# Kernel tuning notes

Hardware: AMD Instinct MI355X
Metric: run time of the kernel (lower is better)

The kernel has to match this reference:

```python
import jax, jax.numpy as jnp
import numpy as np

K = 16
RADIUS = 0.5
LOSS_NORM = 1


def setup_inputs() -> dict:
    key = jax.random.key(0)
    k1, k2 = jax.random.split(key)
    B, N = 2, 8192
    pc = jax.random.normal(k1, (B, N, 3), dtype=jnp.float32)
    flow = jax.random.normal(k2, (B, N, 3), dtype=jnp.float32)
    return {"pc": pc, "flow": flow}


def _ball_query(pc, radius, k):
    """pc: (B,N,3) -> idx (B,N,k) int32. For each query point, the first k
    (in index order) points within radius; empty slots padded with the first
    found index (the query point itself is always in-ball at distance 0),
    matching the pointnet2 CUDA ball_query semantics."""
    B, N, _ = pc.shape
    sq = jnp.sum(pc * pc, axis=-1)  # (B,N)
    # squared pairwise distances via gram matrix: (B,N,N)
    d2 = sq[:, :, None] + sq[:, None, :] - 2.0 * jnp.einsum("bnd,bmd->bnm", pc, pc)
    within = d2 < (radius * radius)
    j = jnp.arange(N, dtype=jnp.int32)
    sentinel = jnp.int32(-2 * N)
    # key = -j for in-ball points, sentinel otherwise; top_k picks smallest j first
    keys = jnp.where(within, -j, sentinel)  # (B,N,N)
    vals, _ = jax.lax.top_k(keys, k)  # (B,N,k)
    idx = -vals
    valid = idx < N
    idx = jnp.where(valid, idx, idx[..., :1])  # pad with first neighbor (self)
    return idx


def reference(pc, flow):
    idx = _ball_query(pc, RADIUS, K)  # (B,N,K)
    # gather neighbor flows: (B,N,K,3)
    nn_flow = jax.vmap(lambda f, i: f[i])(flow, idx)
    diff = flow[:, :, None, :] - nn_flow  # (B,N,K,3)
    if LOSS_NORM == 1:
        norms = jnp.sum(jnp.abs(diff), axis=-1)
    else:
        norms = jnp.sqrt(jnp.sum(diff * diff, axis=-1))
    return jnp.mean(norms)
```

## Files before the change

### kernel.cpp

```cpp
#include <hip/hip_runtime.h>
#include <hip/hip_fp16.h>


#define NQ   8192
#define NB   2
#define KNN  16
#define QPB  64
#define WAVES 8
#define THREADS (QPB * WAVES)
#define NBQ (NB * NQ)
#define GROUPS (NBQ / QPB)
#define SLICES 4
#define SL_PAIRS 1024
#define WPP 128
#define IDXROW 130

static __device__ __forceinline__ unsigned pkrtz_u(float a, float b) {
    return __builtin_bit_cast(unsigned, __builtin_amdgcn_cvt_pkrtz(a, b));
}
static __device__ __forceinline__ __half2 u_as_h2(unsigned u) {
    return __builtin_bit_cast(__half2, u);
}
static __device__ __forceinline__ void bq_pair(unsigned xu, unsigned yu,
                                               unsigned zu, unsigned cu,
                                               __half2 qpx, __half2 qpy,
                                               __half2 qpz, __half2 q2p,
                                               unsigned& mm) {
    __half2 acc = __hsub2(u_as_h2(cu), q2p);
    acc = __hfma2(u_as_h2(xu), qpx, acc);
    acc = __hfma2(u_as_h2(yu), qpy, acc);
    acc = __hfma2(u_as_h2(zu), qpz, acc);
    mm = (__builtin_bit_cast(unsigned, acc) & 0x80008000u) | (mm >> 1);
}

__global__ __launch_bounds__(THREADS, 8)
void ballq_scan(const float* __restrict__ pc,
                unsigned short* __restrict__ wsIdx,
                unsigned char* __restrict__ wsCnt)
{
    __shared__ __align__(16) unsigned lx[SL_PAIRS];
    __shared__ __align__(16) unsigned ly[SL_PAIRS];
    __shared__ __align__(16) unsigned lz[SL_PAIRS];
    __shared__ __align__(16) unsigned lc[SL_PAIRS];
    __shared__ unsigned short s_idx[QPB][IDXROW];
    __shared__ unsigned char  s_cnt[QPB][12];

    const int tid = threadIdx.x;
    const int q   = tid & 63;
    const int c   = tid >> 6;
    const int s   = blockIdx.x & 3;
    const int g   = blockIdx.x >> 2;
    const int b   = g >> 7;
    const int i   = (g & 127) * QPB + q;

    const float* __restrict__ pcb = pc + (size_t)b * NQ * 3;
    const float2* __restrict__ f2 = (const float2*)pcb;

    for (int p = tid; p < SL_PAIRS; p += THREADS) {
        const int gp = s * SL_PAIRS + p;
        const float2 v0 = f2[3 * gp + 0];
        const float2 v1 = f2[3 * gp + 1];
        const float2 v2 = f2[3 * gp + 2];
        lx[p] = pkrtz_u(v0.x, v1.y);
        ly[p] = pkrtz_u(v0.y, v2.x);
        lz[p] = pkrtz_u(v1.x, v2.y);
        const float ne = v0.x * v0.x + v0.y * v0.y + v1.x * v1.x;
        const float no = v1.y * v1.y + v2.x * v2.x + v2.y * v2.y;
        lc[p] = pkrtz_u(0.125f - 0.5f * ne, 0.125f - 0.5f * no);
    }

    const float qx = pcb[i * 3 + 0];
    const float qy = pcb[i * 3 + 1];
    const float qz = pcb[i * 3 + 2];
    const __half2 qpx = u_as_h2(pkrtz_u(qx, qx));
    const __half2 qpy = u_as_h2(pkrtz_u(qy, qy));
    const __half2 qpz = u_as_h2(pkrtz_u(qz, qz));
    const float q2 = 0.5f * (qx * qx + qy * qy + qz * qz);
    const __half2 q2p = u_as_h2(pkrtz_u(q2, q2));

    __syncthreads();

    int cnt = 0;
    for (int r = 0; r < WPP / 64 && cnt < KNN; ++r) {
        const int pbase = c * WPP + r * 64;
        unsigned m[4] = {0u, 0u, 0u, 0u};
#pragma unroll
        for (int g4 = 0; g4 < 4; ++g4) {
#pragma unroll
            for (int w = 0; w < 4; ++w) {
                const int pb = pbase + w * 16 + g4 * 4;
                const uint4 X = *(const uint4*)&lx[pb];
                const uint4 Y = *(const uint4*)&ly[pb];
                const uint4 Z = *(const uint4*)&lz[pb];
                const uint4 C = *(const uint4*)&lc[pb];
                bq_pair(X.x, Y.x, Z.x, C.x, qpx, qpy, qpz, q2p, m[w]);
                bq_pair(X.y, Y.y, Z.y, C.y, qpx, qpy, qpz, q2p, m[w]);
                bq_pair(X.z, Y.z, Z.z, C.z, qpx, qpy, qpz, q2p, m[w]);
                bq_pair(X.w, Y.w, Z.w, C.w, qpx, qpy, qpz, q2p, m[w]);
            }
        }
        if ((m[0] & m[1] & m[2] & m[3]) == 0xFFFFFFFFu) continue;
        const unsigned h0 = ~m[0], h1 = ~m[1], h2m = ~m[2], h3 = ~m[3];

        unsigned long long ev =
              (unsigned long long)(h0 & 0xFFFFu)
            | ((unsigned long long)(h1 & 0xFFFFu) << 16)
            | ((unsigned long long)(h2m & 0xFFFFu) << 32)
            | ((unsigned long long)(h3 & 0xFFFFu) << 48);
        unsigned long long od =
              (unsigned long long)(h0 >> 16)
            | ((unsigned long long)(h1 >> 16) << 16)
            | ((unsigned long long)(h2m >> 16) << 32)
            | ((unsigned long long)(h3 >> 16) << 48);

        const int jb = s * (2 * SL_PAIRS) + 2 * pbase;
        while ((ev | od) && cnt < KNN) {
            const int pe = ev ? __builtin_ctzll(ev) : 127;
            const int po = od ? __builtin_ctzll(od) : 127;
            int j;
            if (pe <= po) { j = jb + 2 * pe;     ev &= ev - 1; }
            else          { j = jb + 2 * po + 1; od &= od - 1; }
            s_idx[q][c * KNN + cnt] = (unsigned short)j;
            ++cnt;
        }
    }
    s_cnt[q][c] = (unsigned char)cnt;
    __syncthreads();

    if (c == 0) {
        const int qid = g * QPB + q;
        unsigned short* __restrict__ rp =
            wsIdx + ((size_t)s * NBQ + qid) * KNN;
        int outc = 0;
        for (int c2 = 0; c2 < WAVES && outc < KNN; ++c2) {
            const int f = s_cnt[q][c2];
            const int take = f < (KNN - outc) ? f : (KNN - outc);
            for (int t = 0; t < take; ++t)
                rp[outc++] = s_idx[q][c2 * KNN + t];
        }
        wsCnt[qid * 4 + s] = (unsigned char)outc;
    }
}

__global__ __launch_bounds__(256)
void ballq_loss(const float* __restrict__ flow,
                const unsigned short* __restrict__ wsIdx,
                const unsigned char* __restrict__ wsCnt,
                float* __restrict__ partial)
{
    const int tid = blockIdx.x * 256 + threadIdx.x;
    const int qid = tid >> 4;
    const int t   = tid & 15;
    const int b   = qid >> 13;
    const int iq  = qid & (NQ - 1);
    const float* __restrict__ flb = flow + (size_t)b * NQ * 3;

    const unsigned cw = *(const unsigned*)(wsCnt + qid * 4);
    const int b0 = cw & 0xFF;
    const int b1 = (cw >> 8)  & 0xFF;
    const int b2 = (cw >> 16) & 0xFF;
    const int c1 = b0, c2c = b0 + b1, c3 = b0 + b1 + b2;
    int tot = c3 + ((cw >> 24) & 0xFF);
    if (tot > KNN) tot = KNN;

    const int seff = (t < tot) ? t : 0;
    const int sl   = (seff >= c1) + (seff >= c2c) + (seff >= c3);
    const int cum  = (sl == 0) ? 0 : (sl == 1) ? c1 : (sl == 2) ? c2c : c3;
    int j = wsIdx[((size_t)sl * NBQ + qid) * KNN + (seff - cum)];
    if (tot == 0) j = iq;

    const float fx = flb[iq * 3 + 0];
    const float fy = flb[iq * 3 + 1];
    const float fz = flb[iq * 3 + 2];
    float l = fabsf(fx - flb[j * 3 + 0]) +
              fabsf(fy - flb[j * 3 + 1]) +
              fabsf(fz - flb[j * 3 + 2]);

    for (int o = 32; o > 0; o >>= 1)
        l += __shfl_down(l, o, 64);
    __shared__ float sred[4];
    if ((threadIdx.x & 63) == 0) sred[threadIdx.x >> 6] = l;
    __syncthreads();
    if (threadIdx.x == 0)
        partial[blockIdx.x] = sred[0] + sred[1] + sred[2] + sred[3];
}

__global__ __launch_bounds__(1024)
void ballq_final(const float* __restrict__ partial, float* __restrict__ out)
{
    const int tid = threadIdx.x;
    float v = partial[tid];
    for (int o = 32; o > 0; o >>= 1)
        v += __shfl_down(v, o, 64);
    __shared__ float s[16];
    if ((tid & 63) == 0) s[tid >> 6] = v;
    __syncthreads();
    if (tid == 0) {
        float t = 0.0f;
#pragma unroll
        for (int w = 0; w < 16; ++w) t += s[w];
        out[0] = t * (1.0f / ((float)NB * NQ * KNN));
    }
}

extern "C" void kernel_launch(void* const* d_in, const int* in_sizes, int n_in,
                              void* d_out, int out_size, void* d_ws, size_t ws_size,
                              hipStream_t stream)
{
    (void)in_sizes; (void)n_in; (void)out_size; (void)ws_size;
    const float* pc   = (const float*)d_in[0];
    const float* flow = (const float*)d_in[1];
    float* out = (float*)d_out;

    unsigned short* wsIdx = (unsigned short*)d_ws;
    unsigned char*  wsCnt = (unsigned char*)d_ws + (size_t)SLICES * NBQ * KNN * 2;
    float* partial = (float*)(wsCnt + (size_t)NBQ * 4);

    ballq_scan<<<GROUPS * SLICES, THREADS, 0, stream>>>(pc, wsIdx, wsCnt);
    ballq_loss<<<NBQ * 16 / 256, 256, 0, stream>>>(flow, wsIdx, wsCnt, partial);
    ballq_final<<<1, 1024, 0, stream>>>(partial, out);
}
```

Before: 33.47 us.

## Transpose ball-query scan: lanes hold candidates, broadcast queries via readlane and ballot

Changes the scan so each lane keeps two candidate point pairs in registers and loops over the 64 queries of its wave, broadcasting each query with readlane and collecting in-ball masks with ballot. Each lane keeps the mask for its own query. This drops the shared-memory staging of candidates and the early-exit per 64-point round, and removes LDS reads from the inner loop. In exchange it always runs all 64 query iterations with two ballots per candidate word and per-lane select bookkeeping, so it loses the chance to stop scanning once 16 neighbors are found.

```diff
diff --git a/kernel.cpp b/kernel.cpp
--- a/kernel.cpp
+++ b/kernel.cpp
@@ -21,122 +21,104 @@
 static __device__ __forceinline__ __half2 u_as_h2(unsigned u) {
     return __builtin_bit_cast(__half2, u);
 }
-static __device__ __forceinline__ void bq_pair(unsigned xu, unsigned yu,
-                                               unsigned zu, unsigned cu,
-                                               __half2 qpx, __half2 qpy,
-                                               __half2 qpz, __half2 q2p,
-                                               unsigned& mm) {
-    __half2 acc = __hsub2(u_as_h2(cu), q2p);
-    acc = __hfma2(u_as_h2(xu), qpx, acc);
-    acc = __hfma2(u_as_h2(yu), qpy, acc);
-    acc = __hfma2(u_as_h2(zu), qpz, acc);
-    mm = (__builtin_bit_cast(unsigned, acc) & 0x80008000u) | (mm >> 1);
-}
 
 __global__ __launch_bounds__(THREADS, 8)
 void ballq_scan(const float* __restrict__ pc,
                 unsigned short* __restrict__ wsIdx,
                 unsigned char* __restrict__ wsCnt)
 {
-    __shared__ __align__(16) unsigned lx[SL_PAIRS];
-    __shared__ __align__(16) unsigned ly[SL_PAIRS];
-    __shared__ __align__(16) unsigned lz[SL_PAIRS];
-    __shared__ __align__(16) unsigned lc[SL_PAIRS];
     __shared__ unsigned short s_idx[QPB][IDXROW];
     __shared__ unsigned char  s_cnt[QPB][12];
 
     const int tid = threadIdx.x;
-    const int q   = tid & 63;
+    const int l   = tid & 63;
     const int c   = tid >> 6;
     const int s   = blockIdx.x & 3;
     const int g   = blockIdx.x >> 2;
     const int b   = g >> 7;
-    const int i   = (g & 127) * QPB + q;
 
     const float* __restrict__ pcb = pc + (size_t)b * NQ * 3;
     const float2* __restrict__ f2 = (const float2*)pcb;
 
-    for (int p = tid; p < SL_PAIRS; p += THREADS) {
-        const int gp = s * SL_PAIRS + p;
-        const float2 v0 = f2[3 * gp + 0];
-        const float2 v1 = f2[3 * gp + 1];
-        const float2 v2 = f2[3 * gp + 2];
-        lx[p] = pkrtz_u(v0.x, v1.y);
-        ly[p] = pkrtz_u(v0.y, v2.x);
-        lz[p] = pkrtz_u(v1.x, v2.y);
-        const float ne = v0.x * v0.x + v0.y * v0.y + v1.x * v1.x;
-        const float no = v1.y * v1.y + v2.x * v2.x + v2.y * v2.y;
-        lc[p] = pkrtz_u(0.125f - 0.5f * ne, 0.125f - 0.5f * no);
-    }
-
+    const int i = (g & 127) * QPB + l;
     const float qx = pcb[i * 3 + 0];
     const float qy = pcb[i * 3 + 1];
     const float qz = pcb[i * 3 + 2];
-    const __half2 qpx = u_as_h2(pkrtz_u(qx, qx));
-    const __half2 qpy = u_as_h2(pkrtz_u(qy, qy));
-    const __half2 qpz = u_as_h2(pkrtz_u(qz, qz));
-    const float q2 = 0.5f * (qx * qx + qy * qy + qz * qz);
-    const __half2 q2p = u_as_h2(pkrtz_u(q2, q2));
-
-    __syncthreads();
+    const unsigned Qx = pkrtz_u(qx, qx);
+    const unsigned Qy = pkrtz_u(qy, qy);
+    const unsigned Qz = pkrtz_u(qz, qz);
+    const float q2f = 0.5f * (qx * qx + qy * qy + qz * qz);
+    const unsigned Q2 = pkrtz_u(q2f, q2f);
+
+    const int pbase = s * SL_PAIRS + c * WPP;
+    unsigned X[2], Y[2], Z[2], C[2];
+#pragma unroll
+    for (int w = 0; w < 2; ++w) {
+        const int p = pbase + w * 64 + l;
+        const float2 v0 = f2[3 * p + 0];
+        const float2 v1 = f2[3 * p + 1];
+        const float2 v2 = f2[3 * p + 2];
+        X[w] = pkrtz_u(v0.x, v1.y);
+        Y[w] = pkrtz_u(v0.y, v2.x);
+        Z[w] = pkrtz_u(v1.x, v2.y);
+        const float ne = v0.x * v0.x + v0.y * v0.y + v1.x * v1.x;
+        const float no = v1.y * v1.y + v2.x * v2.x + v2.y * v2.y;
+        C[w] = pkrtz_u(0.125f - 0.5f * ne, 0.125f - 0.5f * no);
+    }
+
+    unsigned mevlo[2] = {0u, 0u}, mevhi[2] = {0u, 0u};
+    unsigned modlo[2] = {0u, 0u}, modhi[2] = {0u, 0u};
+    for (int qq = 0; qq < 64; ++qq) {
+        const unsigned sqx = (unsigned)__builtin_amdgcn_readlane((int)Qx, qq);
+        const unsigned sqy = (unsigned)__builtin_amdgcn_readlane((int)Qy, qq);
+        const unsigned sqz = (unsigned)__builtin_amdgcn_readlane((int)Qz, qq);
+        const unsigned sq2 = (unsigned)__builtin_amdgcn_readlane((int)Q2, qq);
+        const bool own = (l == qq);
+#pragma unroll
+        for (int w = 0; w < 2; ++w) {
+            __half2 acc = __hsub2(u_as_h2(C[w]), u_as_h2(sq2));
+            acc = __hfma2(u_as_h2(X[w]), u_as_h2(sqx), acc);
+            acc = __hfma2(u_as_h2(Y[w]), u_as_h2(sqy), acc);
+            acc = __hfma2(u_as_h2(Z[w]), u_as_h2(sqz), acc);
+            const int ai = (int)__builtin_bit_cast(unsigned, acc);
+            const unsigned long long hev = __ballot((ai << 16) >= 0);
+            const unsigned long long hod = __ballot(ai >= 0);
+            mevlo[w] = own ? (unsigned)hev         : mevlo[w];
+            mevhi[w] = own ? (unsigned)(hev >> 32) : mevhi[w];
+            modlo[w] = own ? (unsigned)hod         : modlo[w];
+            modhi[w] = own ? (unsigned)(hod >> 32) : modhi[w];
+        }
+    }
 
     int cnt = 0;
-    for (int r = 0; r < WPP / 64 && cnt < KNN; ++r) {
-        const int pbase = c * WPP + r * 64;
-        unsigned m[4] = {0u, 0u, 0u, 0u};
-#pragma unroll
-        for (int g4 = 0; g4 < 4; ++g4) {
-#pragma unroll
-            for (int w = 0; w < 4; ++w) {
-                const int pb = pbase + w * 16 + g4 * 4;
-                const uint4 X = *(const uint4*)&lx[pb];
-                const uint4 Y = *(const uint4*)&ly[pb];
-                const uint4 Z = *(const uint4*)&lz[pb];
-                const uint4 C = *(const uint4*)&lc[pb];
-                bq_pair(X.x, Y.x, Z.x, C.x, qpx, qpy, qpz, q2p, m[w]);
-                bq_pair(X.y, Y.y, Z.y, C.y, qpx, qpy, qpz, q2p, m[w]);
-                bq_pair(X.z, Y.z, Z.z, C.z, qpx, qpy, qpz, q2p, m[w]);
-                bq_pair(X.w, Y.w, Z.w, C.w, qpx, qpy, qpz, q2p, m[w]);
-            }
-        }
-        if ((m[0] & m[1] & m[2] & m[3]) == 0xFFFFFFFFu) continue;
-        const unsigned h0 = ~m[0], h1 = ~m[1], h2m = ~m[2], h3 = ~m[3];
-
-        unsigned long long ev =
-              (unsigned long long)(h0 & 0xFFFFu)
-            | ((unsigned long long)(h1 & 0xFFFFu) << 16)
-            | ((unsigned long long)(h2m & 0xFFFFu) << 32)
-            | ((unsigned long long)(h3 & 0xFFFFu) << 48);
-        unsigned long long od =
-              (unsigned long long)(h0 >> 16)
-            | ((unsigned long long)(h1 >> 16) << 16)
-            | ((unsigned long long)(h2m >> 16) << 32)
-            | ((unsigned long long)(h3 >> 16) << 48);
-
-        const int jb = s * (2 * SL_PAIRS) + 2 * pbase;
+#pragma unroll
+    for (int w = 0; w < 2; ++w) {
+        unsigned long long ev = ((unsigned long long)mevhi[w] << 32) | mevlo[w];
+        unsigned long long od = ((unsigned long long)modhi[w] << 32) | modlo[w];
+        const int jb = 2 * (pbase + w * 64);
         while ((ev | od) && cnt < KNN) {
             const int pe = ev ? __builtin_ctzll(ev) : 127;
             const int po = od ? __builtin_ctzll(od) : 127;
             int j;
             if (pe <= po) { j = jb + 2 * pe;     ev &= ev - 1; }
             else          { j = jb + 2 * po + 1; od &= od - 1; }
-            s_idx[q][c * KNN + cnt] = (unsigned short)j;
+            s_idx[l][c * KNN + cnt] = (unsigned short)j;
             ++cnt;
         }
     }
-    s_cnt[q][c] = (unsigned char)cnt;
+    s_cnt[l][c] = (unsigned char)cnt;
     __syncthreads();
 
     if (c == 0) {
-        const int qid = g * QPB + q;
+        const int qid = g * QPB + l;
         unsigned short* __restrict__ rp =
             wsIdx + ((size_t)s * NBQ + qid) * KNN;
         int outc = 0;
         for (int c2 = 0; c2 < WAVES && outc < KNN; ++c2) {
-            const int f = s_cnt[q][c2];
+            const int f = s_cnt[l][c2];
             const int take = f < (KNN - outc) ? f : (KNN - outc);
             for (int t = 0; t < take; ++t)
-                rp[outc++] = s_idx[q][c2 * KNN + t];
+                rp[outc++] = s_idx[l][c2 * KNN + t];
         }
         wsCnt[qid * 4 + s] = (unsigned char)outc;
     }
@@ -172,14 +154,14 @@
     const float fx = flb[iq * 3 + 0];
     const float fy = flb[iq * 3 + 1];
     const float fz = flb[iq * 3 + 2];
-    float l = fabsf(fx - flb[j * 3 + 0]) +
-              fabsf(fy - flb[j * 3 + 1]) +
-              fabsf(fz - flb[j * 3 + 2]);
+    float lo = fabsf(fx - flb[j * 3 + 0]) +
+               fabsf(fy - flb[j * 3 + 1]) +
+               fabsf(fz - flb[j * 3 + 2]);
 
     for (int o = 32; o > 0; o >>= 1)
-        l += __shfl_down(l, o, 64);
+        lo += __shfl_down(lo, o, 64);
     __shared__ float sred[4];
-    if ((threadIdx.x & 63) == 0) sred[threadIdx.x >> 6] = l;
+    if ((threadIdx.x & 63) == 0) sred[threadIdx.x >> 6] = lo;
     __syncthreads();
     if (threadIdx.x == 0)
         partial[blockIdx.x] = sred[0] + sred[1] + sred[2] + sred[3];
```

New measurement: 53.76 us. +60.6%, slower.
